# Optimization experiments

Measured on AMD Instinct MI355X. Metric: run time of the kernel, lower is better.

The kernel has to match this reference:

```python
import jax, jax.numpy as jnp
import numpy as np

B, S, K, E, H = 64, 25, 20, 256, 8
D = 2 * E  # MHA embed dim (item emb concat user emb)


def setup_inputs() -> dict:
    key = jax.random.key(0)
    ks = jax.random.split(key, 10)
    def w(k, shp, scale=0.02):
        return jax.random.normal(k, shp, jnp.float32) * scale
    return dict(
        item_embs=jax.random.normal(ks[0], (B, S, K, E), jnp.float32),
        user_embs=jax.random.normal(ks[1], (B, E), jnp.float32),
        responses=jax.random.randint(ks[2], (B, S, K), 0, 2),
        Wq=w(ks[3], (D, D)), bq=jnp.zeros((D,), jnp.float32),
        Wk=w(ks[4], (D, D)), bk=jnp.zeros((D,), jnp.float32),
        Wv=w(ks[5], (D, D)), bv=jnp.zeros((D,), jnp.float32),
        Wo=w(ks[6], (D, D)), bo=jnp.zeros((D,), jnp.float32),
        ln_g=jnp.ones((D,), jnp.float32), ln_b=jnp.zeros((D,), jnp.float32),
        W1=w(ks[7], (D, D)), b1=jnp.zeros((D,), jnp.float32),
        W2=w(ks[8], (1, D)), b2=jnp.zeros((1,), jnp.float32),
    )


def _scot_forward(item_embs, user_embs, responses, Wq, bq, Wk, bk, Wv, bv,
                  Wo, bo, ln_g, ln_b, W1, b1, W2, b2):
    Bt, St, Kt, Et = item_embs.shape
    Dt = 2 * Et
    L = St * Kt + 1  # all slate items + prepended zero item
    hd = Dt // H
    # stack_embeddings: concat item emb with broadcast user emb -> [B,S,K,2E]
    x = jnp.concatenate(
        [item_embs, jnp.broadcast_to(user_embs[:, None, None, :], (Bt, St, Kt, Et))], -1)
    x = x.reshape(Bt, St * Kt, Dt)
    # add_zero_item: prepend an all-zero token (slate number 0)
    x = jnp.concatenate([jnp.zeros((Bt, 1, Dt), x.dtype), x], axis=1)  # [B,L,D]
    # slate number per token: 0 for zero item, then 1..S repeated slate_size times
    slateno = jnp.concatenate(
        [jnp.zeros((1,), jnp.int32),
         jnp.repeat(jnp.arange(1, St + 1, dtype=jnp.int32), Kt)])  # [L]
    # clicked mask (zero item counts as clicked) -> keys visible to attention
    clicked = jnp.concatenate(
        [jnp.ones((Bt, 1), bool), responses.reshape(Bt, St * Kt) > 0], axis=1)  # [B,L]
    # attn_mask in the original blocks slateno_q <= slateno_k, except column 0;
    # combined with key_padding over non-clicked keys this equals:
    base_allow = slateno[:, None] > slateno[None, :]
    base_allow = base_allow.at[:, 0].set(True)            # zero item always visible
    allow = base_allow[None, :, :] & clicked[:, None, :]  # [B,L,L]
    # torch MultiheadAttention (batch_first)
    def heads(h):
        return h.reshape(Bt, L, H, hd).transpose(0, 2, 1, 3)  # [B,H,L,hd]
    q = heads(x @ Wq.T + bq)
    k = heads(x @ Wk.T + bk)
    v = heads(x @ Wv.T + bv)
    scores = jnp.einsum('bhqd,bhkd->bhqk', q, k) / np.sqrt(hd).astype(np.float32)
    scores = jnp.where(allow[:, None, :, :], scores, -jnp.inf)
    attn = jax.nn.softmax(scores, axis=-1)
    f = jnp.einsum('bhqk,bhkd->bhqd', attn, v)
    f = f.transpose(0, 2, 1, 3).reshape(Bt, L, Dt) @ Wo.T + bo
    f = f[:, 1:, :]  # drop zero-item query
    # out head: LayerNorm -> Linear -> GELU(exact) -> Linear
    mu = f.mean(-1, keepdims=True)
    var = ((f - mu) ** 2).mean(-1, keepdims=True)
    f = (f - mu) / jnp.sqrt(var + 1e-5) * ln_g + ln_b
    h = jax.nn.gelu(f @ W1.T + b1, approximate=False)
    out = h @ W2.T + b2  # [B, S*K, 1]
    return out.reshape(Bt, St, Kt)


def reference(item_embs, user_embs, responses, Wq, bq, Wk, bk, Wv, bv,
              Wo, bo, ln_g, ln_b, W1, b1, W2, b2):
    return _scot_forward(item_embs, user_embs, responses, Wq, bq, Wk, bk,
                         Wv, bv, Wo, bo, ln_g, ln_b, W1, b1, W2, b2)
```

## Files before the change

kernel.cpp:

```cpp
#include <hip/hip_runtime.h>
#include <math.h>

#define BATCH 64
#define SLATES 25
#define KPS 20
#define EDIM 256
#define DDIM 512
#define HEADS 8
#define HD 64
#define LFULL 501
#define NROWS 500
#define MTOT (BATCH*NROWS)
#define CMAX 512
#define NQKV 1536

typedef __attribute__((ext_vector_type(8))) short short8;
typedef __attribute__((ext_vector_type(4))) float f32x4;

__device__ __forceinline__ unsigned short f2bf(float x) {
    unsigned int u = __builtin_bit_cast(unsigned int, x);
    u = (u + 0x7FFFu + ((u >> 16) & 1u)) >> 16;
    return (unsigned short)u;
}
__device__ __forceinline__ float bf2f(unsigned short s) {
    unsigned int u = ((unsigned int)s) << 16;
    return __builtin_bit_cast(float, u);
}
__device__ __forceinline__ float gelu_exact(float x) {
    return 0.5f * x * (1.0f + erff(x * 0.70710678118654752440f));
}
__device__ __forceinline__ void gload16(const void* g, void* l) {
    __builtin_amdgcn_global_load_lds(
        (const __attribute__((address_space(1))) void*)g,
        (__attribute__((address_space(3))) void*)l, 16, 0, 0);
}

__global__ __launch_bounds__(256) void cvt_kernel(
    const float* __restrict__ src, unsigned short* __restrict__ dst, int n4)
{
    const int i = blockIdx.x * 256 + threadIdx.x;
    if (i >= n4) return;
    float4 v = ((const float4*)src)[i];
    ushort4 o;
    o.x = f2bf(v.x); o.y = f2bf(v.y); o.z = f2bf(v.z); o.w = f2bf(v.w);
    ((ushort4*)dst)[i] = o;
}

struct Cvt2 { const float* s[2]; unsigned short* d[2]; };
__global__ __launch_bounds__(256) void cvt2_kernel(Cvt2 a, int n4)
{
    const int i = blockIdx.x * 256 + threadIdx.x;
    if (i >= n4) return;
    const int y = blockIdx.y;
    float4 v = ((const float4*)a.s[y])[i];
    ushort4 o;
    o.x = f2bf(v.x); o.y = f2bf(v.y); o.z = f2bf(v.z); o.w = f2bf(v.w);
    ((ushort4*)a.d[y])[i] = o;
}

__global__ __launch_bounds__(256) void packqkv_kernel(
    const float* __restrict__ Wq, const float* __restrict__ Wk,
    const float* __restrict__ Wv, unsigned short* __restrict__ dst)
{
    const int y = blockIdx.y;
    const float* W = (y == 0) ? Wq : (y == 1) ? Wk : Wv;
    const int i = blockIdx.x * 256 + threadIdx.x;
    const int row = i >> 6, c4 = (i & 63) * 4;
    float4 v = *(const float4*)&W[(size_t)row * DDIM + c4];
    ushort4 o;
    o.x = f2bf(v.x); o.y = f2bf(v.y); o.z = f2bf(v.z); o.w = f2bf(v.w);
    *(ushort4*)&dst[((size_t)y * DDIM + row) * EDIM + c4] = o;
}

__global__ __launch_bounds__(64) void compact_kernel(
    const int* __restrict__ resp, int* __restrict__ cidx, int* __restrict__ cnt)
{
    const int b = blockIdx.x, lane = threadIdx.x;
    int a[8]; int c = 0;
#pragma unroll
    for (int j = 0; j < 8; ++j) {
        const int l = lane * 8 + j;
        int al = 0;
        if (l == 0) al = 1;
        else if (l <= NROWS) al = (resp[(size_t)b * NROWS + l - 1] > 0) ? 1 : 0;
        a[j] = al; c += al;
    }
    int incl = c;
#pragma unroll
    for (int off = 1; off < 64; off <<= 1) {
        int t = __shfl_up(incl, off, 64);
        if (lane >= off) incl += t;
    }
    int run = incl - c;
#pragma unroll
    for (int j = 0; j < 8; ++j) {
        const int l = lane * 8 + j;
        if (l >= 1 && l <= 481 && (l % 20) == 1)
            cnt[b * 32 + (l - 1) / 20] = run;
        cidx[b * 512 + l] = a[j] ? run : -1;
        run += a[j];
    }
}

__global__ __launch_bounds__(256) void user_bias_kernel(
    const float* __restrict__ user,
    const float* __restrict__ Wq, const float* __restrict__ bq,
    const float* __restrict__ Wk, const float* __restrict__ bk,
    const float* __restrict__ Wv, const float* __restrict__ bv,
    float* __restrict__ uball,
    unsigned short* __restrict__ qb, unsigned short* __restrict__ kc,
    unsigned short* __restrict__ vc)
{
    const int b = blockIdx.x;
    const int y = blockIdx.y;
    const int tid = threadIdx.x;
    const float* W  = (y == 0) ? Wq : (y == 1) ? Wk : Wv;
    const float* bi = (y == 0) ? bq : (y == 1) ? bk : bv;

    __shared__ float us[EDIM];
    if (tid < EDIM) us[tid] = user[b * EDIM + tid];
    __syncthreads();
    for (int o = tid; o < DDIM; o += 256) {
        float s = bi[o];
        const float* wr = &W[(size_t)o * DDIM + EDIM];
#pragma unroll 4
        for (int e = 0; e < EDIM; ++e) s += us[e] * wr[e];
        uball[(size_t)b * NQKV + y * DDIM + o] = s;
        const int hh = o >> 6, dd = o & 63;
        const size_t bh = (size_t)b * HEADS + hh;
        if (y == 0)      qb[(bh * LFULL) * HD + dd] = f2bf(bi[o]);
        else if (y == 1) kc[(bh * CMAX) * HD + dd] = f2bf(bi[o]);
        else             vc[(bh * HD + dd) * CMAX] = f2bf(bi[o]);
    }
}

__global__ __launch_bounds__(256) void gemm_qkv(
    const unsigned short* __restrict__ A,
    const unsigned short* __restrict__ Wqkv,
    const float* __restrict__ uball, const int* __restrict__ cidx,
    unsigned short* __restrict__ oq, unsigned short* __restrict__ ok,
    unsigned short* __restrict__ ov)
{
    const int tid = threadIdx.x;
    const int lin = blockIdx.y * gridDim.x + blockIdx.x;
    const int vb  = (lin & 7) * 375 + (lin >> 3);
    const int n0 = (vb % 12) * 128;
    const int m0 = (vb / 12) * 128;
    const int lane = tid & 63, wid = tid >> 6;
    const int wm = (wid & 1) * 64, wn = (wid >> 1) * 64;

    __shared__ __align__(16) unsigned short sm[24576];
    __shared__ int cids[128];
    auto As = [&](int buf) { return (unsigned short(*)[32])(sm + buf * 4096); };
    auto Ws = [&](int buf) { return (unsigned short(*)[32])(sm + 12288 + buf * 4096); };
    auto bounce = (unsigned short(*)[136])sm;

    f32x4 acc[4][4];
#pragma unroll
    for (int i = 0; i < 4; ++i)
#pragma unroll
        for (int j = 0; j < 4; ++j) acc[i][j] = (f32x4){0.f, 0.f, 0.f, 0.f};

    const unsigned short* gA0 = &A[(size_t)(m0 + wid * 16 + (lane >> 2)) * EDIM + (lane & 3) * 8];
    const unsigned short* gA1 = gA0 + (size_t)64 * EDIM;
    const unsigned short* gW0 = &Wqkv[(size_t)(n0 + wid * 16 + (lane >> 2)) * EDIM + (lane & 3) * 8];
    const unsigned short* gW1 = gW0 + (size_t)64 * EDIM;
    const int frow = lane & 15, fk = (lane >> 4) * 8;

    auto stage = [&](int buf, int k0) {
        gload16(gA0 + k0, &As(buf)[wid * 16][0]);
        gload16(gA1 + k0, &As(buf)[64 + wid * 16][0]);
        gload16(gW0 + k0, &Ws(buf)[wid * 16][0]);
        gload16(gW1 + k0, &Ws(buf)[64 + wid * 16][0]);
    };
    stage(0, 0);
    stage(1, 32);

    const int nst = EDIM / 32;
    for (int t = 0; t < nst; ++t) {
        const int cur = t % 3;
        if (t < nst - 1) asm volatile("s_waitcnt vmcnt(4)" ::: "memory");
        else             asm volatile("s_waitcnt vmcnt(0)" ::: "memory");
        __builtin_amdgcn_s_barrier();
        __builtin_amdgcn_sched_barrier(0);
        short8 af[4], wf[4];
#pragma unroll
        for (int mi = 0; mi < 4; ++mi)
            af[mi] = *(const short8*)&As(cur)[wm + mi * 16 + frow][fk];
#pragma unroll
        for (int ni = 0; ni < 4; ++ni)
            wf[ni] = *(const short8*)&Ws(cur)[wn + ni * 16 + frow][fk];
#pragma unroll
        for (int mi = 0; mi < 4; ++mi)
#pragma unroll
            for (int ni = 0; ni < 4; ++ni)
                acc[mi][ni] = __builtin_amdgcn_mfma_f32_16x16x32_bf16(
                    af[mi], wf[ni], acc[mi][ni], 0, 0, 0);
        if (t + 2 < nst) stage((t + 2) % 3, (t + 2) * 32);
    }

    const int z = n0 >> 9;
    const int b0 = m0 / NROWS;
    const int split = (b0 + 1) * NROWS;
    const int b1 = (split <= m0 + 127) ? b0 + 1 : b0;
    float ub0[4], ub1[4];
#pragma unroll
    for (int ni = 0; ni < 4; ++ni) {
        const int np = n0 + wn + ni * 16 + frow;
        ub0[ni] = uball[(size_t)b0 * NQKV + np];
        ub1[ni] = uball[(size_t)b1 * NQKV + np];
    }
    __syncthreads();
    if (z != 0 && tid < 128) {
        const int m = m0 + tid;
        const int b = (m >= split) ? b1 : b0;
        cids[tid] = cidx[b * 512 + (m - b * NROWS + 1)];
    }
#pragma unroll
    for (int mi = 0; mi < 4; ++mi)
#pragma unroll
        for (int r = 0; r < 4; ++r) {
            const int ml = wm + mi * 16 + (lane >> 4) * 4 + r;
            const bool hi = (m0 + ml >= split);
#pragma unroll
            for (int ni = 0; ni < 4; ++ni)
                bounce[ml][wn + ni * 16 + frow] =
                    f2bf(acc[mi][ni][r] + (hi ? ub1[ni] : ub0[ni]));
        }
    __syncthreads();

    const int h0 = (n0 & 511) >> 6;
    if (z == 0) {
        const int row = tid >> 1, half = tid & 1;
        const int m = m0 + row;
        const int b = (m >= split) ? b1 : b0;
        const int l = m - b * NROWS + 1;
        unsigned short* dst = &oq[(((size_t)b * HEADS + h0 + half) * LFULL + l) * HD];
        const unsigned short* src = &bounce[row][half * 64];
#pragma unroll
        for (int j = 0; j < 8; ++j)
            *(uint4*)(dst + j * 8) = *(const uint4*)(src + j * 8);
    } else if (z == 1) {
        const int row = tid >> 1, half = tid & 1;
        const int c = cids[row];
        if (c >= 0) {
            const int m = m0 + row;
            const int b = (m >= split) ? b1 : b0;
            unsigned short* dst = &ok[(((size_t)b * HEADS + h0 + half) * CMAX + c) * HD];
            const unsigned short* src = &bounce[row][half * 64];
#pragma unroll
            for (int j = 0; j < 8; ++j)
                *(uint4*)(dst + j * 8) = *(const uint4*)(src + j * 8);
        }
    } else {
        const int col = tid & 127, mh = tid >> 7;
        const int hh = h0 + (col >> 6), dd = col & 63;
        for (int mm = 0; mm < 64; ++mm) {
            const int row = mh * 64 + mm;
            const int c = cids[row];
            if (c >= 0) {
                const int m = m0 + row;
                const int b = (m >= split) ? b1 : b0;
                ov[((size_t)b * HEADS + hh) * (size_t)(HD * CMAX)
                   + (size_t)dd * CMAX + c] = bounce[row][col];
            }
        }
    }
}

template <int MODE>
__global__ __launch_bounds__(256) void gemm_bf16(
    const unsigned short* __restrict__ A,
    const unsigned short* __restrict__ W,
    const float* __restrict__ bias, void* __restrict__ outp,
    const float* __restrict__ W2, float* __restrict__ part)
{
    const int tid = threadIdx.x;
    const int lin = blockIdx.y * gridDim.x + blockIdx.x;
    const int vb  = (lin & 7) * 125 + (lin >> 3);
    const int n0 = (vb % 4) * 128;
    const int m0 = (vb / 4) * 128;
    const int lane = tid & 63, wid = tid >> 6;
    const int wm = (wid & 1) * 64, wn = (wid >> 1) * 64;

    __shared__ unsigned short As[3][128][32];
    __shared__ unsigned short Ws[3][128][32];

    f32x4 acc[4][4];
#pragma unroll
    for (int i = 0; i < 4; ++i)
#pragma unroll
        for (int j = 0; j < 4; ++j) acc[i][j] = (f32x4){0.f, 0.f, 0.f, 0.f};

    const unsigned short* gA0 = &A[(size_t)(m0 + wid * 16 + (lane >> 2)) * DDIM + (lane & 3) * 8];
    const unsigned short* gA1 = gA0 + (size_t)64 * DDIM;
    const unsigned short* gW0 = &W[(size_t)(n0 + wid * 16 + (lane >> 2)) * DDIM + (lane & 3) * 8];
    const unsigned short* gW1 = gW0 + (size_t)64 * DDIM;
    const int frow = lane & 15, fk = (lane >> 4) * 8;

    auto stage = [&](int buf, int k0) {
        gload16(gA0 + k0, &As[buf][wid * 16][0]);
        gload16(gA1 + k0, &As[buf][64 + wid * 16][0]);
        gload16(gW0 + k0, &Ws[buf][wid * 16][0]);
        gload16(gW1 + k0, &Ws[buf][64 + wid * 16][0]);
    };
    stage(0, 0);
    stage(1, 32);

    const int nst = DDIM / 32;
    for (int t = 0; t < nst; ++t) {
        const int cur = t % 3;
        if (t < nst - 1) asm volatile("s_waitcnt vmcnt(4)" ::: "memory");
        else             asm volatile("s_waitcnt vmcnt(0)" ::: "memory");
        __builtin_amdgcn_s_barrier();
        __builtin_amdgcn_sched_barrier(0);
        short8 af[4], wf[4];
#pragma unroll
        for (int mi = 0; mi < 4; ++mi)
            af[mi] = *(const short8*)&As[cur][wm + mi * 16 + frow][fk];
#pragma unroll
        for (int ni = 0; ni < 4; ++ni)
            wf[ni] = *(const short8*)&Ws[cur][wn + ni * 16 + frow][fk];
#pragma unroll
        for (int mi = 0; mi < 4; ++mi)
#pragma unroll
            for (int ni = 0; ni < 4; ++ni)
                acc[mi][ni] = __builtin_amdgcn_mfma_f32_16x16x32_bf16(
                    af[mi], wf[ni], acc[mi][ni], 0, 0, 0);
        if (t + 2 < nst) stage((t + 2) % 3, (t + 2) * 32);
    }

    if (MODE == 1) {
#pragma unroll
        for (int mi = 0; mi < 4; ++mi)
#pragma unroll
            for (int ni = 0; ni < 4; ++ni) {
                const int n = n0 + wn + ni * 16 + frow;
                const float bv = bias[n];
#pragma unroll
                for (int r = 0; r < 4; ++r) {
                    const int m = m0 + wm + mi * 16 + (lane >> 4) * 4 + r;
                    ((unsigned short*)outp)[(size_t)m * DDIM + n] =
                        f2bf(acc[mi][ni][r] + bv);
                }
            }
    } else {
        float w2v[4], bv4[4];
#pragma unroll
        for (int ni = 0; ni < 4; ++ni) {
            const int n = n0 + wn + ni * 16 + frow;
            w2v[ni] = W2[n];
            bv4[ni] = bias[n];
        }
        float ps[4][4];
#pragma unroll
        for (int mi = 0; mi < 4; ++mi)
#pragma unroll
            for (int r = 0; r < 4; ++r) ps[mi][r] = 0.f;
#pragma unroll
        for (int mi = 0; mi < 4; ++mi)
#pragma unroll
            for (int ni = 0; ni < 4; ++ni)
#pragma unroll
                for (int r = 0; r < 4; ++r)
                    ps[mi][r] += gelu_exact(acc[mi][ni][r] + bv4[ni]) * w2v[ni];
        const int slot = (n0 >> 7) * 2 + (wn >> 6);
#pragma unroll
        for (int mi = 0; mi < 4; ++mi)
#pragma unroll
            for (int r = 0; r < 4; ++r) {
                float s = ps[mi][r];
                s += __shfl_xor(s, 1, 64);
                s += __shfl_xor(s, 2, 64);
                s += __shfl_xor(s, 4, 64);
                s += __shfl_xor(s, 8, 64);
                if (frow == 0) {
                    const int m = m0 + wm + mi * 16 + (lane >> 4) * 4 + r;
                    part[(size_t)m * 8 + slot] = s;
                }
            }
    }
}

__global__ __launch_bounds__(256) void w2red_kernel(
    const float* __restrict__ part, const float* __restrict__ b2,
    float* __restrict__ out)
{
    const int m = blockIdx.x * 256 + threadIdx.x;
    if (m >= MTOT) return;
    const float* p = part + (size_t)m * 8;
    float s = b2[0];
#pragma unroll
    for (int i = 0; i < 8; ++i) s += p[i];
    out[m] = s;
}

__global__ __launch_bounds__(256) void attn_mfma(
    const unsigned short* __restrict__ qx, const unsigned short* __restrict__ kc,
    const unsigned short* __restrict__ vc, const int* __restrict__ cnt,
    unsigned short* __restrict__ outb)
{
    const int lin = blockIdx.x + SLATES * (blockIdx.y + HEADS * blockIdx.z);
    const int vbk = (lin & 7) * 1600 + (lin >> 3);
    const int s0 = vbk % SLATES;
    const int h  = (vbk / SLATES) % HEADS;
    const int b  = vbk / (SLATES * HEADS);

    const int tid = threadIdx.x, lane = tid & 63, w = tid >> 6;
    const int nck = cnt[b * 32 + s0];
    const int NT = (nck + 63) >> 6;

    __shared__ __align__(16) unsigned short scb[KPS][520];
    __shared__ float rsw[4][32];

    const int frow = lane & 15, fk = (lane >> 4) * 8;
    const size_t bh = (size_t)b * HEADS + h;
    const unsigned short* kbase = kc + bh * (CMAX * HD);
    const unsigned short* vbase = vc + bh * (HD * CMAX);

    short8 qf[2][2];
#pragma unroll
    for (int mi = 0; mi < 2; ++mi) {
        const int qrow = mi * 16 + frow;
#pragma unroll
        for (int ks = 0; ks < 2; ++ks) {
            short8 v = {};
            if (qrow < KPS)
                v = *(const short8*)&qx[(bh * LFULL + s0 * KPS + 1 + qrow) * HD
                                        + ks * 32 + fk];
            qf[mi][ks] = v;
        }
    }

    f32x4 rsum[2];
    rsum[0] = (f32x4){0.f, 0.f, 0.f, 0.f};
    rsum[1] = (f32x4){0.f, 0.f, 0.f, 0.f};
    for (int t = 0; t < NT; ++t) {
        const int key = (t << 6) + w * 16 + frow;
        const unsigned short* kr = kbase + (size_t)key * HD;
        const short8 kf0 = *(const short8*)(kr + fk);
        const short8 kf1 = *(const short8*)(kr + 32 + fk);
        f32x4 s2[2];
#pragma unroll
        for (int mi = 0; mi < 2; ++mi) {
            s2[mi] = (f32x4){0.f, 0.f, 0.f, 0.f};
            s2[mi] = __builtin_amdgcn_mfma_f32_16x16x32_bf16(qf[mi][0], kf0, s2[mi], 0, 0, 0);
            s2[mi] = __builtin_amdgcn_mfma_f32_16x16x32_bf16(qf[mi][1], kf1, s2[mi], 0, 0, 0);
        }
        const bool allow = key < nck;
#pragma unroll
        for (int mi = 0; mi < 2; ++mi)
#pragma unroll
            for (int r = 0; r < 4; ++r) {
                const int row = mi * 16 + (lane >> 4) * 4 + r;
                const float p = allow ? __expf(s2[mi][r] * 0.125f) : 0.f;
                rsum[mi][r] += p;
                if (row < KPS)
                    scb[row][key] = f2bf(p);
            }
    }
#pragma unroll
    for (int mi = 0; mi < 2; ++mi)
#pragma unroll
        for (int r = 0; r < 4; ++r) {
            float v = rsum[mi][r];
            v += __shfl_xor(v, 1, 64);
            v += __shfl_xor(v, 2, 64);
            v += __shfl_xor(v, 4, 64);
            v += __shfl_xor(v, 8, 64);
            if (frow == 0)
                rsw[w][mi * 16 + (lane >> 4) * 4 + r] = v;
        }
    __syncthreads();

    f32x4 po[2];
    po[0] = (f32x4){0.f, 0.f, 0.f, 0.f};
    po[1] = (f32x4){0.f, 0.f, 0.f, 0.f};
    const unsigned short* vrow = vbase + (size_t)(w * 16 + frow) * CMAX;
    for (int t = 0; t < NT; ++t) {
#pragma unroll
        for (int ks = 0; ks < 2; ++ks) {
            const int kb0 = (t << 6) + ks * 32 + fk;
            short8 vf;
            if (t + 1 < NT || kb0 + 8 <= nck) {
                vf = *(const short8*)(vrow + kb0);
            } else {
#pragma unroll
                for (int j = 0; j < 8; ++j)
                    vf[j] = (kb0 + j < nck) ? (short)vrow[kb0 + j] : (short)0;
            }
#pragma unroll
            for (int mi = 0; mi < 2; ++mi) {
                short8 pf = {};
                const int prow = mi * 16 + frow;
                if (prow < KPS)
                    pf = *(const short8*)&scb[prow][kb0];
                po[mi] = __builtin_amdgcn_mfma_f32_16x16x32_bf16(pf, vf, po[mi], 0, 0, 0);
            }
        }
    }

#pragma unroll
    for (int mi = 0; mi < 2; ++mi)
#pragma unroll
        for (int r = 0; r < 4; ++r) {
            const int row = mi * 16 + (lane >> 4) * 4 + r;
            if (row < KPS) {
                const float inv = 1.0f / (rsw[0][row] + rsw[1][row]
                                        + rsw[2][row] + rsw[3][row]);
                outb[((size_t)b * NROWS + s0 * KPS + row) * DDIM
                     + h * HD + w * 16 + frow] = f2bf(po[mi][r] * inv);
            }
        }
}

__global__ __launch_bounds__(256) void ln_kernel(
    const unsigned short* __restrict__ f, const float* __restrict__ g,
    const float* __restrict__ bt, unsigned short* __restrict__ o)
{
    const int row = blockIdx.x * 4 + (threadIdx.x >> 6);
    const int lane = threadIdx.x & 63;
    const size_t base = (size_t)row * DDIM + lane * 8;
    short8 v = *(const short8*)&f[base];
    float xv[8];
    float s = 0.f;
#pragma unroll
    for (int i = 0; i < 8; ++i) { xv[i] = bf2f((unsigned short)v[i]); s += xv[i]; }
#pragma unroll
    for (int off = 32; off; off >>= 1) s += __shfl_xor(s, off, 64);
    const float mu = s * (1.0f / DDIM);
    float var = 0.f;
#pragma unroll
    for (int i = 0; i < 8; ++i) { const float d0 = xv[i] - mu; var += d0 * d0; }
#pragma unroll
    for (int off = 32; off; off >>= 1) var += __shfl_xor(var, off, 64);
    const float rs = rsqrtf(var * (1.0f / DDIM) + 1e-5f);
    short8 ov;
#pragma unroll
    for (int i = 0; i < 8; ++i) {
        const int d0 = lane * 8 + i;
        ov[i] = (short)f2bf((xv[i] - mu) * rs * g[d0] + bt[d0]);
    }
    *(short8*)&o[base] = ov;
}

extern "C" void kernel_launch(void* const* d_in, const int* in_sizes, int n_in,
                              void* d_out, int out_size, void* d_ws, size_t ws_size,
                              hipStream_t stream)
{
    const float* item = (const float*)d_in[0];
    const float* user = (const float*)d_in[1];
    const int*   resp = (const int*)d_in[2];
    const float* Wq = (const float*)d_in[3];  const float* bq = (const float*)d_in[4];
    const float* Wk = (const float*)d_in[5];  const float* bk = (const float*)d_in[6];
    const float* Wv = (const float*)d_in[7];  const float* bv = (const float*)d_in[8];
    const float* Wo = (const float*)d_in[9];  const float* bo = (const float*)d_in[10];
    const float* lng = (const float*)d_in[11]; const float* lnb = (const float*)d_in[12];
    const float* W1 = (const float*)d_in[13]; const float* b1 = (const float*)d_in[14];
    const float* W2 = (const float*)d_in[15]; const float* b2 = (const float*)d_in[16];
    float* out = (float*)d_out;

    char* p = (char*)d_ws;
    auto alloc = [&](size_t bytes) { char* r = p; p += (bytes + 255) & ~(size_t)255; return r; };
    const size_t NITEM = (size_t)BATCH * NROWS * EDIM;
    const size_t NW    = (size_t)DDIM * DDIM;
    const size_t NQ    = (size_t)BATCH * HEADS * LFULL * HD;
    const size_t NC    = (size_t)BATCH * HEADS * CMAX * HD;
    const size_t NMD   = (size_t)MTOT * DDIM;
    const size_t PAD   = 8192;

    unsigned short* itemb  = (unsigned short*)alloc(NITEM * 2);
    unsigned short* Wqkvb  = (unsigned short*)alloc((size_t)NQKV * EDIM * 2);
    unsigned short* Wob    = (unsigned short*)alloc(NW * 2);
    unsigned short* W1b    = (unsigned short*)alloc(NW * 2);
    unsigned short* qb     = (unsigned short*)alloc(NQ * 2 + PAD);
    unsigned short* kcb    = (unsigned short*)alloc(NC * 2 + PAD);
    unsigned short* vcb    = (unsigned short*)alloc(NC * 2 + PAD);
    unsigned short* aob    = (unsigned short*)alloc(NMD * 2);
    unsigned short* fb16   = (unsigned short*)alloc(NMD * 2);
    float* uball = (float*)alloc((size_t)BATCH * NQKV * 4);
    float* part  = (float*)alloc((size_t)MTOT * 8 * 4);
    int* cidx    = (int*)alloc((size_t)BATCH * 512 * 4);
    int* cnt     = (int*)alloc((size_t)BATCH * 32 * 4);

    cvt_kernel<<<dim3((NITEM / 4 + 255) / 256), 256, 0, stream>>>(item, itemb, NITEM / 4);
    packqkv_kernel<<<dim3(DDIM * EDIM / 4 / 256, 3), 256, 0, stream>>>(Wq, Wk, Wv, Wqkvb);
    Cvt2 c2;
    c2.s[0] = Wo; c2.s[1] = W1; c2.d[0] = Wob; c2.d[1] = W1b;
    cvt2_kernel<<<dim3(NW / 4 / 256, 2), 256, 0, stream>>>(c2, NW / 4);

    compact_kernel<<<dim3(BATCH), 64, 0, stream>>>(resp, cidx, cnt);

    user_bias_kernel<<<dim3(BATCH, 3), 256, 0, stream>>>(
        user, Wq, bq, Wk, bk, Wv, bv, uball, qb, kcb, vcb);

    gemm_qkv<<<dim3(NQKV / 128, MTOT / 128), 256, 0, stream>>>(
        itemb, Wqkvb, uball, cidx, qb, kcb, vcb);

    attn_mfma<<<dim3(SLATES, HEADS, BATCH), 256, 0, stream>>>(qb, kcb, vcb, cnt, aob);

    dim3 gg(DDIM / 128, MTOT / 128);
    gemm_bf16<1><<<gg, 256, 0, stream>>>(aob, Wob, bo, fb16, nullptr, nullptr);
    ln_kernel<<<dim3(MTOT / 4), 256, 0, stream>>>(fb16, lng, lnb, aob);
    gemm_bf16<2><<<gg, 256, 0, stream>>>(aob, W1b, b1, nullptr, W2, part);
    w2red_kernel<<<dim3((MTOT + 255) / 256), 256, 0, stream>>>(part, b2, out);
}
```

Measured before the change: 295.4 us.

## Tile attention by 32-row query blocks across slates with per-row key masks

The attention kernel now gives each block 32 consecutive query rows per (batch, head), which can span slate boundaries. Before, each block handled one slate of 20 rows and left 12 of the 32 MFMA rows unused. Each row gets its own visible-key count from shared memory. The loop bound comes from the last row's count, which assumes counts rise with slate index. The guarded tail loads of V are dropped, so padded V entries beyond the count are read unconditionally. This is correct only if those entries hold finite values, since they are multiplied by zero probabilities.

Result: faster. 280.7 us (-5.0%).

```diff
diff --git a/kernel.cpp b/kernel.cpp
--- a/kernel.cpp
+++ b/kernel.cpp
@@ -13,6 +13,8 @@
 #define MTOT (BATCH*NROWS)
 #define CMAX 512
 #define NQKV 1536
+#define RB 32
+#define NRB ((NROWS + RB - 1) / RB)
 
 typedef __attribute__((ext_vector_type(8))) short short8;
 typedef __attribute__((ext_vector_type(4))) float f32x4;
@@ -400,37 +402,51 @@
     const unsigned short* __restrict__ vc, const int* __restrict__ cnt,
     unsigned short* __restrict__ outb)
 {
-    const int lin = blockIdx.x + SLATES * (blockIdx.y + HEADS * blockIdx.z);
-    const int vbk = (lin & 7) * 1600 + (lin >> 3);
-    const int s0 = vbk % SLATES;
-    const int h  = (vbk / SLATES) % HEADS;
-    const int b  = vbk / (SLATES * HEADS);
+    const int lin = blockIdx.x + NRB * (blockIdx.y + HEADS * blockIdx.z);
+    const int vbk = (lin & 7) * (NRB * HEADS * BATCH / 8) + (lin >> 3);
+    const int rbk = vbk % NRB;
+    const int h   = (vbk / NRB) % HEADS;
+    const int b   = vbk / (NRB * HEADS);
+    const int g0  = rbk * RB;
 
     const int tid = threadIdx.x, lane = tid & 63, w = tid >> 6;
-    const int nck = cnt[b * 32 + s0];
-    const int NT = (nck + 63) >> 6;
-
-    __shared__ __align__(16) unsigned short scb[KPS][520];
-    __shared__ float rsw[4][32];
+
+    __shared__ __align__(16) unsigned short scb[RB][520];
+    __shared__ float rsw[4][RB];
+    __shared__ int snck[RB];
 
     const int frow = lane & 15, fk = (lane >> 4) * 8;
     const size_t bh = (size_t)b * HEADS + h;
     const unsigned short* kbase = kc + bh * (CMAX * HD);
     const unsigned short* vbase = vc + bh * (HD * CMAX);
 
+    if (tid < RB) {
+        const int s = (g0 + tid >= NROWS ? NROWS - 1 : g0 + tid) / KPS;
+        snck[tid] = cnt[b * 32 + s];
+    }
+
     short8 qf[2][2];
 #pragma unroll
     for (int mi = 0; mi < 2; ++mi) {
-        const int qrow = mi * 16 + frow;
+        const int qrow = g0 + mi * 16 + frow;
 #pragma unroll
         for (int ks = 0; ks < 2; ++ks) {
             short8 v = {};
-            if (qrow < KPS)
-                v = *(const short8*)&qx[(bh * LFULL + s0 * KPS + 1 + qrow) * HD
-                                        + ks * 32 + fk];
+            if (qrow < NROWS)
+                v = *(const short8*)&qx[(bh * LFULL + qrow + 1) * HD + ks * 32 + fk];
             qf[mi][ks] = v;
         }
     }
+    __syncthreads();
+
+    int nck8[2][4];
+#pragma unroll
+    for (int mi = 0; mi < 2; ++mi)
+#pragma unroll
+        for (int r = 0; r < 4; ++r)
+            nck8[mi][r] = snck[mi * 16 + (lane >> 4) * 4 + r];
+    const int nmax = snck[RB - 1];
+    const int NT = (nmax + 63) >> 6;
 
     f32x4 rsum[2];
     rsum[0] = (f32x4){0.f, 0.f, 0.f, 0.f};
@@ -447,16 +463,14 @@
             s2[mi] = __builtin_amdgcn_mfma_f32_16x16x32_bf16(qf[mi][0], kf0, s2[mi], 0, 0, 0);
             s2[mi] = __builtin_amdgcn_mfma_f32_16x16x32_bf16(qf[mi][1], kf1, s2[mi], 0, 0, 0);
         }
-        const bool allow = key < nck;
 #pragma unroll
         for (int mi = 0; mi < 2; ++mi)
 #pragma unroll
             for (int r = 0; r < 4; ++r) {
                 const int row = mi * 16 + (lane >> 4) * 4 + r;
-                const float p = allow ? __expf(s2[mi][r] * 0.125f) : 0.f;
+                const float p = (key < nck8[mi][r]) ? __expf(s2[mi][r] * 0.125f) : 0.f;
                 rsum[mi][r] += p;
-                if (row < KPS)
-                    scb[row][key] = f2bf(p);
+                scb[row][key] = f2bf(p);
             }
     }
 #pragma unroll
@@ -481,20 +495,10 @@
 #pragma unroll
         for (int ks = 0; ks < 2; ++ks) {
             const int kb0 = (t << 6) + ks * 32 + fk;
-            short8 vf;
-            if (t + 1 < NT || kb0 + 8 <= nck) {
-                vf = *(const short8*)(vrow + kb0);
-            } else {
-#pragma unroll
-                for (int j = 0; j < 8; ++j)
-                    vf[j] = (kb0 + j < nck) ? (short)vrow[kb0 + j] : (short)0;
-            }
+            const short8 vf = *(const short8*)(vrow + kb0);
 #pragma unroll
             for (int mi = 0; mi < 2; ++mi) {
-                short8 pf = {};
-                const int prow = mi * 16 + frow;
-                if (prow < KPS)
-                    pf = *(const short8*)&scb[prow][kb0];
+                const short8 pf = *(const short8*)&scb[mi * 16 + frow][kb0];
                 po[mi] = __builtin_amdgcn_mfma_f32_16x16x32_bf16(pf, vf, po[mi], 0, 0, 0);
             }
         }
@@ -505,10 +509,11 @@
 #pragma unroll
         for (int r = 0; r < 4; ++r) {
             const int row = mi * 16 + (lane >> 4) * 4 + r;
-            if (row < KPS) {
+            const int m = g0 + row;
+            if (m < NROWS) {
                 const float inv = 1.0f / (rsw[0][row] + rsw[1][row]
                                         + rsw[2][row] + rsw[3][row]);
-                outb[((size_t)b * NROWS + s0 * KPS + row) * DDIM
+                outb[((size_t)b * NROWS + m) * DDIM
                      + h * HD + w * 16 + frow] = f2bf(po[mi][r] * inv);
             }
         }
@@ -597,7 +602,7 @@
     gemm_qkv<<<dim3(NQKV / 128, MTOT / 128), 256, 0, stream>>>(
         itemb, Wqkvb, uball, cidx, qb, kcb, vcb);
 
-    attn_mfma<<<dim3(SLATES, HEADS, BATCH), 256, 0, stream>>>(qb, kcb, vcb, cnt, aob);
+    attn_mfma<<<dim3(NRB, HEADS, BATCH), 256, 0, stream>>>(qb, kcb, vcb, cnt, aob);
 
     dim3 gg(DDIM / 128, MTOT / 128);
     gemm_bf16<1><<<gg, 256, 0, stream>>>(aob, Wob, bo, fb16, nullptr, nullptr);
```
